# Performance work log

Hardware: AMD Instinct MI355X
Metric: run time of the kernel (lower is better)

The kernel has to match this reference:

```python
import jax, jax.numpy as jnp
import numpy as np

D_MODEL = 1024
NUM_HEADS = 16
DEPTH = D_MODEL // NUM_HEADS
NEG_INF = -1e9


def setup_inputs() -> dict:
    key = jax.random.key(0)
    ks = jax.random.split(key, 12)
    B, S = 4, 2048
    scale = 1.0 / np.sqrt(D_MODEL)
    inp = {
        "q": jax.random.normal(ks[0], (B, S, D_MODEL), jnp.float32),
        "k": jax.random.normal(ks[1], (B, S, D_MODEL), jnp.float32),
        "v": jax.random.normal(ks[2], (B, S, D_MODEL), jnp.float32),
        "mask": jax.random.randint(ks[3], (B, 1, 1, S), 0, 2, jnp.int32),
        "wq": jax.random.normal(ks[4], (D_MODEL, D_MODEL), jnp.float32) * scale,
        "bq": jnp.zeros((D_MODEL,), jnp.float32),
        "wk": jax.random.normal(ks[5], (D_MODEL, D_MODEL), jnp.float32) * scale,
        "bk": jnp.zeros((D_MODEL,), jnp.float32),
        "wv": jax.random.normal(ks[6], (D_MODEL, D_MODEL), jnp.float32) * scale,
        "bv": jnp.zeros((D_MODEL,), jnp.float32),
        "wo": jax.random.normal(ks[7], (D_MODEL, D_MODEL), jnp.float32) * scale,
        "bo": jnp.zeros((D_MODEL,), jnp.float32),
    }
    return inp


def _split_heads(x):
    # [B, S, D] -> [B, H, S, depth]
    B, S, _ = x.shape
    return x.reshape(B, S, NUM_HEADS, DEPTH).transpose(0, 2, 1, 3)


def reference(q, k, v, mask, wq, bq, wk, bk, wv, bv, wo, bo):
    B, S, _ = q.shape
    qh = _split_heads(q @ wq + bq)  # [B,H,S,d]
    kh = _split_heads(k @ wk + bk)
    vh = _split_heads(v @ wv + bv)
    logits = jnp.einsum("bhqd,bhkd->bhqk", qh, kh) / jnp.sqrt(
        jnp.asarray(DEPTH, jnp.float32))
    logits = logits + mask.astype(jnp.float32) * NEG_INF
    weights = jax.nn.softmax(logits, axis=-1)
    attn = jnp.einsum("bhqk,bhkd->bhqd", weights, vh)
    attn = attn.transpose(0, 2, 1, 3).reshape(B, S, D_MODEL)
    return attn @ wo + bo
```

## Files before the change

kernel.cpp:

```cpp
#include <hip/hip_runtime.h>

#define SB 4
#define SS 2048
#define SD 1024
#define SH 16

typedef float f32x4 __attribute__((ext_vector_type(4)));
typedef __bf16 bf16x8 __attribute__((ext_vector_type(8)));
typedef short short4v __attribute__((ext_vector_type(4)));
typedef unsigned int uint2v __attribute__((ext_vector_type(2)));

__device__ __forceinline__ unsigned short f2bf_(float x) {
    unsigned u = __builtin_bit_cast(unsigned, x);
    unsigned r = u + 0x7FFFu + ((u >> 16) & 1u);
    return (unsigned short)(r >> 16);
}

#define GL2LDS(g, l) __builtin_amdgcn_global_load_lds( \
    (const __attribute__((address_space(1))) unsigned int*)(g), \
    (__attribute__((address_space(3))) unsigned int*)(l), 16, 0, 0)

__global__ __launch_bounds__(256) void maskprep(
        const int* __restrict__ mk, float* __restrict__ MA, int n) {
    int i = blockIdx.x * 256 + threadIdx.x;
    if (i < n)
        MA[i] = (float)mk[i] * (-1e9f * 1.4426950408889634f) - 8.0f;
}

__global__ __launch_bounds__(256) void transpose4(
        const float* __restrict__ w0, const float* __restrict__ w1,
        const float* __restrict__ w2, const float* __restrict__ w3,
        unsigned short* __restrict__ out) {
    __shared__ unsigned short tile[32][33];
    int zz = blockIdx.z;
    const float* src = (zz == 0) ? w0 : (zz == 1) ? w1 : (zz == 2) ? w2 : w3;
    unsigned short* dst = out + (size_t)zz * 1024 * 1024;
    int x = blockIdx.x * 32 + threadIdx.x;
    int y0 = blockIdx.y * 32;
    for (int j = threadIdx.y; j < 32; j += 8)
        tile[j][threadIdx.x] = f2bf_(src[(size_t)(y0 + j) * 1024 + x]);
    __syncthreads();
    int ox = y0 + threadIdx.x;
    int oy0 = blockIdx.x * 32;
    for (int j = threadIdx.y; j < 32; j += 8)
        dst[(size_t)(oy0 + j) * 1024 + ox] = tile[threadIdx.x][j];
}

__global__ __launch_bounds__(512) void gemm_qkv(
        const float* __restrict__ Aq, const float* __restrict__ Ak,
        const float* __restrict__ Avv, const unsigned short* __restrict__ WT,
        const float* __restrict__ bq, const float* __restrict__ bk,
        const float* __restrict__ bv, unsigned short* __restrict__ Qh,
        unsigned short* __restrict__ Kh, unsigned short* __restrict__ VTr,
        float qscl) {
    const int K = 1024, N = 1024;
    __shared__ alignas(16) float Asmf[2][128][32];
    __shared__ alignas(16) unsigned short Bsm[2][128][32];
    const int zone = blockIdx.z;
    const float* Af = (zone == 0) ? Aq : (zone == 1) ? Ak : Avv;
    const unsigned short* BT = WT + (size_t)zone * 1048576;
    const float* bias = (zone == 0) ? bq : (zone == 1) ? bk : bv;

    const int m0 = blockIdx.x * 128, n0 = blockIdx.y * 128;
    const int lane = threadIdx.x & 63, wid = threadIdx.x >> 6;
    const int wr = wid >> 2, wc = wid & 3;
    const int cl = lane & 15, kg = lane >> 4;

    f32x4 acc[4][2] = {};

    auto STAGE = [&](int buf, int k0) {
#pragma unroll
        for (int i = 0; i < 2; ++i) {
            int base = i * 64 + wid * 8;
            int row = base + (lane >> 3);
            int cs = (lane & 7) ^ (row & 7);
            GL2LDS(Af + (size_t)(m0 + row) * K + k0 + cs * 4, &Asmf[buf][base][0]);
        }
        {
            int base = wid * 16;
            int row = base + (lane >> 2);
            int cs = (lane & 3) ^ ((row >> 1) & 3);
            GL2LDS(BT + (size_t)(n0 + row) * K + k0 + cs * 8, &Bsm[buf][base][0]);
        }
    };

    STAGE(0, 0);
    __syncthreads();

    for (int k0 = 0; k0 < K; k0 += 32) {
        int cur = (k0 >> 5) & 1;
        if (k0 + 32 < K) STAGE(cur ^ 1, k0 + 32);

        bf16x8 af[4], bfv[2];
#pragma unroll
        for (int mi = 0; mi < 4; ++mi) {
            int r = wr * 64 + mi * 16 + cl;
            const float* Ar = &Asmf[cur][r][0];
            f32x4 a0 = *(const f32x4*)(Ar + ((2 * kg) ^ (r & 7)) * 4);
            f32x4 a1 = *(const f32x4*)(Ar + ((2 * kg + 1) ^ (r & 7)) * 4);
#pragma unroll
            for (int e = 0; e < 4; ++e) {
                af[mi][e] = (__bf16)a0[e];
                af[mi][4 + e] = (__bf16)a1[e];
            }
        }
#pragma unroll
        for (int ni = 0; ni < 2; ++ni) {
            int r = wc * 32 + ni * 16 + cl;
            bfv[ni] = *(const bf16x8*)&Bsm[cur][r][(kg ^ ((r >> 1) & 3)) * 8];
        }
#pragma unroll
        for (int mi = 0; mi < 4; ++mi)
#pragma unroll
            for (int ni = 0; ni < 2; ++ni)
                acc[mi][ni] = __builtin_amdgcn_mfma_f32_16x16x32_bf16(
                    af[mi], bfv[ni], acc[mi][ni], 0, 0, 0);
        __syncthreads();
    }

    const int rl = (lane >> 4) * 4;
    float os = (zone == 0) ? qscl : 1.0f;
#pragma unroll
    for (int mi = 0; mi < 4; ++mi) {
#pragma unroll
        for (int ni = 0; ni < 2; ++ni) {
            int row = m0 + wr * 64 + mi * 16 + rl;
            int col = n0 + wc * 32 + ni * 16 + cl;
            float bvv = bias[col];
            f32x4 v = acc[mi][ni];
            if (zone < 2) {
                unsigned short* C = (zone == 0) ? Qh : Kh;
#pragma unroll
                for (int j = 0; j < 4; ++j)
                    C[(size_t)(row + j) * N + col] = f2bf_((v[j] + bvv) * os);
            } else {
                int bb = row >> 11, s = row & 2047;
                short4v pk;
#pragma unroll
                for (int j = 0; j < 4; ++j)
                    pk[j] = (short)f2bf_(v[j] + bvv);
                *(short4v*)&VTr[((size_t)(bb * 1024 + col)) * 2048 + s] = pk;
            }
        }
    }
}

__global__ __launch_bounds__(256) void gemm_out(
        const unsigned short* __restrict__ Ab, const unsigned short* __restrict__ BT,
        const float* __restrict__ bias, float* __restrict__ C,
        int M, int N, int K) {
    __shared__ alignas(16) unsigned short Asmb[2][128][32];
    __shared__ alignas(16) unsigned short Bsm[2][128][32];
    const int m0 = blockIdx.x * 128, n0 = blockIdx.y * 128;
    const int lane = threadIdx.x & 63, wid = threadIdx.x >> 6;
    const int wr = wid >> 1, wc = wid & 1;
    const int cl = lane & 15, kg = lane >> 4;

    f32x4 acc[4][4] = {};

    auto STAGE = [&](int buf, int k0) {
#pragma unroll
        for (int i = 0; i < 2; ++i) {
            int base = (i * 4 + wid) * 16;
            int row = base + (lane >> 2);
            int cs = (lane & 3) ^ ((row >> 1) & 3);
            GL2LDS(Ab + (size_t)(m0 + row) * K + k0 + cs * 8, &Asmb[buf][base][0]);
            GL2LDS(BT + (size_t)(n0 + row) * K + k0 + cs * 8, &Bsm[buf][base][0]);
        }
    };

    STAGE(0, 0);
    __syncthreads();

    for (int k0 = 0; k0 < K; k0 += 32) {
        int cur = (k0 >> 5) & 1;
        if (k0 + 32 < K) STAGE(cur ^ 1, k0 + 32);

        bf16x8 af[4], bfv[4];
#pragma unroll
        for (int mi = 0; mi < 4; ++mi) {
            int r = wr * 64 + mi * 16 + cl;
            af[mi] = *(const bf16x8*)&Asmb[cur][r][(kg ^ ((r >> 1) & 3)) * 8];
        }
#pragma unroll
        for (int ni = 0; ni < 4; ++ni) {
            int r = wc * 64 + ni * 16 + cl;
            bfv[ni] = *(const bf16x8*)&Bsm[cur][r][(kg ^ ((r >> 1) & 3)) * 8];
        }
#pragma unroll
        for (int mi = 0; mi < 4; ++mi)
#pragma unroll
            for (int ni = 0; ni < 4; ++ni)
                acc[mi][ni] = __builtin_amdgcn_mfma_f32_16x16x32_bf16(
                    af[mi], bfv[ni], acc[mi][ni], 0, 0, 0);
        __syncthreads();
    }

    const int rl = (lane >> 4) * 4;
#pragma unroll
    for (int mi = 0; mi < 4; ++mi) {
#pragma unroll
        for (int ni = 0; ni < 4; ++ni) {
            int row = m0 + wr * 64 + mi * 16 + rl;
            int col = n0 + wc * 64 + ni * 16 + cl;
            float bv = bias[col];
            f32x4 v = acc[mi][ni];
#pragma unroll
            for (int j = 0; j < 4; ++j)
                C[(size_t)(row + j) * N + col] = v[j] + bv;
        }
    }
}

__global__ __launch_bounds__(512, 4) void attn_kernel(
        const unsigned short* __restrict__ Qp, const unsigned short* __restrict__ Kp,
        const unsigned short* __restrict__ VT, const float* __restrict__ MA,
        unsigned short* __restrict__ O) {
    __shared__ alignas(16) unsigned short Klds[2][128][64];
    __shared__ alignas(16) unsigned short Vlds[2][64][128];
    const int lane = threadIdx.x & 63, wid = threadIdx.x >> 6;
    const int bh = blockIdx.x;
    const int b = bh >> 4, h = bh & 15;
    const int qt = blockIdx.y;
    const int qrow0 = qt * 256 + wid * 32;
    const int cl = lane & 15, kg = lane >> 4;

    bf16x8 qf[2][2];
#pragma unroll
    for (int qh = 0; qh < 2; ++qh)
#pragma unroll
        for (int kh = 0; kh < 2; ++kh)
            qf[qh][kh] = *(const bf16x8*)&Qp[(size_t)(b * SS + qrow0 + qh * 16 + cl) * SD
                                            + h * 64 + kh * 32 + kg * 8];

    const float* MAb = MA + b * SS;

    bf16x8 onesf;
#pragma unroll
    for (int e = 0; e < 8; ++e) onesf[e] = (__bf16)1.0f;

    f32x4 oacc[2][4] = {};
    f32x4 lacc[2] = {};

    auto STAGE = [&](int buf, int tt) {
        int kt = (tt & 15) * 128;
        {
            int r8 = lane >> 3, c8 = lane & 7;
#pragma unroll
            for (int i = 0; i < 2; ++i) {
                int r = i * 64 + wid * 8 + r8;
                int cs = c8 ^ (r & 7);
                GL2LDS(Kp + (size_t)(b * SS + kt + r) * SD + h * 64 + cs * 8,
                       &Klds[buf][i * 64 + wid * 8][0]);
            }
        }
        {
            int r16 = lane >> 4, c16 = lane & 15;
#pragma unroll
            for (int i = 0; i < 2; ++i) {
                int r = i * 32 + wid * 4 + r16;
                int cs = (c16 & 8) | ((c16 & 7) ^ (r & 7));
                GL2LDS(VT + (size_t)(b * 1024 + h * 64 + r) * 2048 + kt + cs * 8,
                       &Vlds[buf][i * 32 + wid * 4][0]);
            }
        }
    };

    auto QKCOL = [&](int buf, int kt, int cf, f32x4* sv) {
        int r = cf * 16 + cl;
        bf16x8 kf0 = *(const bf16x8*)&Klds[buf][r][((0 + kg) ^ (r & 7)) * 8];
        bf16x8 kf1 = *(const bf16x8*)&Klds[buf][r][((4 + kg) ^ (r & 7)) * 8];
        f32x4 M = *(const f32x4*)&MAb[kt + cf * 16 + 4 * kg];
        __builtin_amdgcn_s_setprio(1);
#pragma unroll
        for (int qh = 0; qh < 2; ++qh) {
            f32x4 s = {};
            s = __builtin_amdgcn_mfma_f32_16x16x32_bf16(kf0, qf[qh][0], s, 0, 0, 0);
            s = __builtin_amdgcn_mfma_f32_16x16x32_bf16(kf1, qf[qh][1], s, 0, 0, 0);
#pragma unroll
            for (int j = 0; j < 4; ++j)
                s[j] = __builtin_amdgcn_exp2f(s[j] + M[j]);
            sv[qh] = s;
        }
        __builtin_amdgcn_s_setprio(0);
    };

    auto STEP = [&](int buf, int t) {
        int kt = t * 128;
#pragma unroll
        for (int ks = 0; ks < 4; ++ks) {
            f32x4 sA[2], sB[2];
            QKCOL(buf, kt, ks, sA);
            QKCOL(buf, kt, ks + 4, sB);
            bf16x8 pa[2];
#pragma unroll
            for (int qh = 0; qh < 2; ++qh) {
                pa[qh][0] = (__bf16)sA[qh][0];
                pa[qh][1] = (__bf16)sA[qh][1];
                pa[qh][2] = (__bf16)sA[qh][2];
                pa[qh][3] = (__bf16)sA[qh][3];
                pa[qh][4] = (__bf16)sB[qh][0];
                pa[qh][5] = (__bf16)sB[qh][1];
                pa[qh][6] = (__bf16)sB[qh][2];
                pa[qh][7] = (__bf16)sB[qh][3];
            }
            __builtin_amdgcn_s_setprio(1);
#pragma unroll
            for (int qh = 0; qh < 2; ++qh)
                lacc[qh] = __builtin_amdgcn_mfma_f32_16x16x32_bf16(
                    pa[qh], onesf, lacc[qh], 0, 0, 0);
#pragma unroll
            for (int nf = 0; nf < 4; ++nf) {
                int d = nf * 16 + cl;
                int c16a = 2 * ks + (kg >> 1);
                int c16b = 2 * (ks + 4) + (kg >> 1);
                int cha = (c16a & 8) | ((c16a & 7) ^ (d & 7));
                int chb = (c16b & 8) | ((c16b & 7) ^ (d & 7));
                const char* vb = (const char*)&Vlds[buf][d][0];
                uint2v lo = *(const uint2v*)(vb + cha * 16 + (kg & 1) * 8);
                uint2v hi = *(const uint2v*)(vb + chb * 16 + (kg & 1) * 8);
                bf16x8 vf;
                *(uint2v*)&vf = lo;
                *((uint2v*)&vf + 1) = hi;
#pragma unroll
                for (int qh = 0; qh < 2; ++qh)
                    oacc[qh][nf] = __builtin_amdgcn_mfma_f32_16x16x32_bf16(
                        pa[qh], vf, oacc[qh][nf], 0, 0, 0);
            }
            __builtin_amdgcn_s_setprio(0);
        }
    };

    STAGE(0, 0);
    __syncthreads();
    for (int t = 0; t < 16; ++t) {
        int cur = t & 1;
        STAGE(cur ^ 1, t + 1);
        STEP(cur, t);
        __syncthreads();
    }

#pragma unroll
    for (int qh = 0; qh < 2; ++qh) {
#pragma unroll
        for (int j = 0; j < 4; ++j) {
            float inv = 1.0f / lacc[qh][j];
#pragma unroll
            for (int nf = 0; nf < 4; ++nf)
                O[(size_t)(b * SS + qrow0 + qh * 16 + 4 * kg + j) * SD + h * 64 + nf * 16 + cl] =
                    f2bf_(oacc[qh][nf][j] * inv);
        }
    }
}

extern "C" void kernel_launch(void* const* d_in, const int* in_sizes, int n_in,
                              void* d_out, int out_size, void* d_ws, size_t ws_size,
                              hipStream_t stream) {
    const float* q  = (const float*)d_in[0];
    const float* k  = (const float*)d_in[1];
    const float* v  = (const float*)d_in[2];
    const int*   mk = (const int*)d_in[3];
    const float* wq = (const float*)d_in[4];
    const float* bq = (const float*)d_in[5];
    const float* wk = (const float*)d_in[6];
    const float* bk = (const float*)d_in[7];
    const float* wv = (const float*)d_in[8];
    const float* bv = (const float*)d_in[9];
    const float* wo = (const float*)d_in[10];
    const float* bo = (const float*)d_in[11];
    float* out = (float*)d_out;

    char* ws = (char*)d_ws;
    unsigned short* WT  = (unsigned short*)ws;
    unsigned short* X   = (unsigned short*)(ws + 8388608);
    unsigned short* Qh  = (unsigned short*)(ws + 25165824);
    unsigned short* Kh  = (unsigned short*)(ws + 41943040);
    unsigned short* VTr = (unsigned short*)(ws + 58720256);
    float*          MAf = (float*)(ws + 75497472);

    const float QSCL = 0.125f * 1.4426950408889634f;

    transpose4<<<dim3(32, 32, 4), dim3(32, 8), 0, stream>>>(wq, wk, wv, wo, WT);
    maskprep<<<dim3(32), dim3(256), 0, stream>>>(mk, MAf, SB * SS);

    gemm_qkv<<<dim3(64, 8, 3), dim3(512), 0, stream>>>(
        q, k, v, WT, bq, bk, bv, Qh, Kh, VTr, QSCL);

    attn_kernel<<<dim3(64, 8), dim3(512), 0, stream>>>(Qh, Kh, VTr, MAf, X);

    gemm_out<<<dim3(64, 8), dim3(256), 0, stream>>>(
        X, WT + 3 * 1048576, bo, out, 8192, 1024, 1024);
}
```

Measured before the change: 192.9 us.

## Convert A tile to bf16 in registers before LDS store in QKV GEMM

The QKV projection GEMM now loads fp32 activation tiles into registers, converts them to bf16 once per element, and writes them to a padded bf16 LDS buffer. Before, the fp32 tiles went straight to LDS and every wave converted them after reading. The main loop is unrolled by two with register prefetch two tiles ahead, so global loads overlap compute. This halves LDS footprint and traffic for A and removes redundant conversions, at the cost of more registers and a register round trip instead of direct global-to-LDS loads.

```diff
diff --git a/kernel.cpp b/kernel.cpp
--- a/kernel.cpp
+++ b/kernel.cpp
@@ -54,7 +54,7 @@
         unsigned short* __restrict__ Kh, unsigned short* __restrict__ VTr,
         float qscl) {
     const int K = 1024, N = 1024;
-    __shared__ alignas(16) float Asmf[2][128][32];
+    __shared__ alignas(16) unsigned short Asm[2][128][40];
     __shared__ alignas(16) unsigned short Bsm[2][128][32];
     const int zone = blockIdx.z;
     const float* Af = (zone == 0) ? Aq : (zone == 1) ? Ak : Avv;
@@ -62,52 +62,46 @@
     const float* bias = (zone == 0) ? bq : (zone == 1) ? bk : bv;
 
     const int m0 = blockIdx.x * 128, n0 = blockIdx.y * 128;
-    const int lane = threadIdx.x & 63, wid = threadIdx.x >> 6;
+    const int tid = threadIdx.x;
+    const int lane = tid & 63, wid = tid >> 6;
     const int wr = wid >> 2, wc = wid & 3;
     const int cl = lane & 15, kg = lane >> 4;
+    const int arow = tid >> 2, aseg = tid & 3;
 
     f32x4 acc[4][2] = {};
-
-    auto STAGE = [&](int buf, int k0) {
-#pragma unroll
-        for (int i = 0; i < 2; ++i) {
-            int base = i * 64 + wid * 8;
-            int row = base + (lane >> 3);
-            int cs = (lane & 7) ^ (row & 7);
-            GL2LDS(Af + (size_t)(m0 + row) * K + k0 + cs * 4, &Asmf[buf][base][0]);
-        }
-        {
-            int base = wid * 16;
-            int row = base + (lane >> 2);
-            int cs = (lane & 3) ^ ((row >> 1) & 3);
-            GL2LDS(BT + (size_t)(n0 + row) * K + k0 + cs * 8, &Bsm[buf][base][0]);
-        }
-    };
-
-    STAGE(0, 0);
-    __syncthreads();
-
-    for (int k0 = 0; k0 < K; k0 += 32) {
-        int cur = (k0 >> 5) & 1;
-        if (k0 + 32 < K) STAGE(cur ^ 1, k0 + 32);
-
+    f32x4 ra0[2], ra1[2];
+
+    auto LOADA = [&](int k0, f32x4* r) {
+        const float* p = Af + (size_t)(m0 + arow) * K + k0 + aseg * 8;
+        r[0] = *(const f32x4*)p;
+        r[1] = *(const f32x4*)(p + 4);
+    };
+    auto WRITEA = [&](int buf, const f32x4* r) {
+        bf16x8 w;
+#pragma unroll
+        for (int e = 0; e < 4; ++e) {
+            w[e] = (__bf16)r[0][e];
+            w[4 + e] = (__bf16)r[1][e];
+        }
+        *(bf16x8*)&Asm[buf][arow][aseg * 8] = w;
+    };
+    auto STAGEB = [&](int buf, int k0) {
+        int base = wid * 16;
+        int row = base + (lane >> 2);
+        int cs = (lane & 3) ^ ((row >> 1) & 3);
+        GL2LDS(BT + (size_t)(n0 + row) * K + k0 + cs * 8, &Bsm[buf][base][0]);
+    };
+    auto COMPUTE = [&](int buf) {
         bf16x8 af[4], bfv[2];
 #pragma unroll
         for (int mi = 0; mi < 4; ++mi) {
             int r = wr * 64 + mi * 16 + cl;
-            const float* Ar = &Asmf[cur][r][0];
-            f32x4 a0 = *(const f32x4*)(Ar + ((2 * kg) ^ (r & 7)) * 4);
-            f32x4 a1 = *(const f32x4*)(Ar + ((2 * kg + 1) ^ (r & 7)) * 4);
-#pragma unroll
-            for (int e = 0; e < 4; ++e) {
-                af[mi][e] = (__bf16)a0[e];
-                af[mi][4 + e] = (__bf16)a1[e];
-            }
+            af[mi] = *(const bf16x8*)&Asm[buf][r][kg * 8];
         }
 #pragma unroll
         for (int ni = 0; ni < 2; ++ni) {
             int r = wc * 32 + ni * 16 + cl;
-            bfv[ni] = *(const bf16x8*)&Bsm[cur][r][(kg ^ ((r >> 1) & 3)) * 8];
+            bfv[ni] = *(const bf16x8*)&Bsm[buf][r][(kg ^ ((r >> 1) & 3)) * 8];
         }
 #pragma unroll
         for (int mi = 0; mi < 4; ++mi)
@@ -115,6 +109,26 @@
             for (int ni = 0; ni < 2; ++ni)
                 acc[mi][ni] = __builtin_amdgcn_mfma_f32_16x16x32_bf16(
                     af[mi], bfv[ni], acc[mi][ni], 0, 0, 0);
+    };
+
+    LOADA(0, ra0);
+    STAGEB(0, 0);
+    WRITEA(0, ra0);
+    LOADA(32, ra1);
+    __syncthreads();
+
+#pragma unroll 1
+    for (int tt = 0; tt < 16; ++tt) {
+        int t0 = 2 * tt;
+        if (t0 + 2 < 32) LOADA(t0 * 32 + 64, ra0);
+        STAGEB(1, t0 * 32 + 32);
+        COMPUTE(0);
+        WRITEA(1, ra1);
+        __syncthreads();
+        if (t0 + 3 < 32) LOADA(t0 * 32 + 96, ra1);
+        if (t0 + 2 < 32) STAGEB(0, t0 * 32 + 64);
+        COMPUTE(1);
+        if (t0 + 2 < 32) WRITEA(0, ra0);
         __syncthreads();
     }
 
```

After: 184.4 us. -4.4%, faster.
